# Kernel tuning notes

Hardware: AMD Instinct MI355X
Metric: run time of the kernel (lower is better)

Reference implementation:

```python
import jax, jax.numpy as jnp
import numpy as np


def _pairwise_sq_dist(a, b):
    # a: (B,N,D), b: (B,M,D) -> (B,N,M) squared euclidean distances
    # matmul trick matching torch.cdist (clamped at 0 before implicit sqrt)
    a2 = jnp.sum(a * a, axis=-1)  # (B,N)
    b2 = jnp.sum(b * b, axis=-1)  # (B,M)
    ab = jnp.einsum('bnd,bmd->bnm', a, b)  # (B,N,M)
    d2 = a2[:, :, None] + b2[:, None, :] - 2.0 * ab
    return jnp.maximum(d2, 0.0)


def setup_inputs() -> dict:
    key = jax.random.key(0)
    k1, k2 = jax.random.split(key)
    B, N, M, D = 8, 8192, 8192, 3
    gts = jax.random.normal(k1, (B, N, D), dtype=jnp.float32)
    preds = jax.random.normal(k2, (B, M, D), dtype=jnp.float32)
    return {"gts": gts, "preds": preds}


def reference(gts, preds):
    d2 = _pairwise_sq_dist(gts, preds)           # (B,N,M)
    min_g2p = jnp.min(d2, axis=2)                # (B,N) nearest pred for each gt
    min_p2g = jnp.min(d2, axis=1)                # (B,M) nearest gt for each pred
    return jnp.mean(min_g2p) + jnp.mean(min_p2g)
```

## Files before the change

kernel.cpp:

```cpp
#include <hip/hip_runtime.h>
#include <math.h>

#define BB 8
#define NN 8192
#define MM 8192

#define ROWS_PER_BLOCK 256
#define COLS_PER_BLOCK 1024
#define NTILES (COLS_PER_BLOCK / 32)

typedef __attribute__((ext_vector_type(8)))  short short8;
typedef __attribute__((ext_vector_type(16))) float float16;

#define ONE_BF16 ((short)0x3F80)

__device__ inline unsigned short bf16rn(float f) {
    unsigned int u = __float_as_uint(f);
    u += 0x7FFFu + ((u >> 16) & 1u);
    return (unsigned short)(u >> 16);
}
__device__ inline float bf2f(unsigned short h) {
    return __uint_as_float(((unsigned int)h) << 16);
}
__device__ inline float min16(const float16 d) {
    float v = fminf(fminf(d[0], d[1]), d[2]);
    v = fminf(fminf(v, d[3]),  d[4]);
    v = fminf(fminf(v, d[5]),  d[6]);
    v = fminf(fminf(v, d[7]),  d[8]);
    v = fminf(fminf(v, d[9]),  d[10]);
    v = fminf(fminf(v, d[11]), d[12]);
    v = fminf(fminf(v, d[13]), d[14]);
    return fminf(v, d[15]);
}


__global__ __launch_bounds__(512, 4) void chamfer_main(
    const float* __restrict__ gts, const float* __restrict__ preds,
    unsigned int* __restrict__ minn, unsigned int* __restrict__ minp)
{
    __shared__ short8 sBlo[COLS_PER_BLOCK];
    __shared__ short8 sBhi[COLS_PER_BLOCK];
    __shared__ int colmin[COLS_PER_BLOCK];

    const int b       = blockIdx.z;
    const int rowBase = blockIdx.x * ROWS_PER_BLOCK;
    const int colBase = blockIdx.y * COLS_PER_BLOCK;
    const int tid  = threadIdx.x;
    const int lane = tid & 63;
    const int wave = tid >> 6;
    const int h    = lane >> 5;
    const int c    = lane & 31;

    for (int i = tid; i < COLS_PER_BLOCK; i += 512) {
        const float* p = preds + ((size_t)b * MM + colBase + i) * 3;
        float x = p[0], y = p[1], z = p[2];
        float w = x * x + y * y + z * z;
        unsigned short xh = bf16rn(x), yh = bf16rn(y), zh = bf16rn(z);
        unsigned short xl = bf16rn(x - bf2f(xh));
        unsigned short yl = bf16rn(y - bf2f(yh));
        unsigned short zl = bf16rn(z - bf2f(zh));
        unsigned short wh = bf16rn(w);
        unsigned short wl = bf16rn(w - bf2f(wh));
        short8 lo, hi;
        lo[0]=(short)xh; lo[1]=(short)yh; lo[2]=(short)zh; lo[3]=(short)xl;
        lo[4]=(short)yl; lo[5]=(short)zl; lo[6]=(short)xh; lo[7]=(short)yh;
        hi[0]=(short)zh; hi[1]=ONE_BF16;  hi[2]=ONE_BF16;  hi[3]=(short)wh;
        hi[4]=(short)wl; hi[5]=0;         hi[6]=0;         hi[7]=0;
        sBlo[i] = lo; sBhi[i] = hi;
        colmin[i] = 0x7F800000;
    }

    const float* g = gts + ((size_t)b * NN + rowBase + wave * 32 + c) * 3;
    float gx = g[0], gy = g[1], gz = g[2];
    float gw = gx * gx + gy * gy + gz * gz;
    float mx = -2.0f * gx, my = -2.0f * gy, mz = -2.0f * gz;
    unsigned short axh = bf16rn(mx), ayh = bf16rn(my), azh = bf16rn(mz);
    unsigned short axl = bf16rn(mx - bf2f(axh));
    unsigned short ayl = bf16rn(my - bf2f(ayh));
    unsigned short azl = bf16rn(mz - bf2f(azh));
    unsigned short awh = bf16rn(gw);
    unsigned short awl = bf16rn(gw - bf2f(awh));
    short8 alo, ahi;
    alo[0]=(short)axh; alo[1]=(short)ayh; alo[2]=(short)azh; alo[3]=(short)axh;
    alo[4]=(short)ayh; alo[5]=(short)azh; alo[6]=(short)axl; alo[7]=(short)ayl;
    ahi[0]=(short)azl; ahi[1]=(short)awh; ahi[2]=(short)awl; ahi[3]=ONE_BF16;
    ahi[4]=ONE_BF16;   ahi[5]=0;          ahi[6]=0;          ahi[7]=0;
    short8 afrag = h ? ahi : alo;

    float16 zacc;
#pragma unroll
    for (int q = 0; q < 16; ++q) zacc[q] = 0.0f;

    const float kInf = __builtin_inff();
    float rm[16];
#pragma unroll
    for (int q = 0; q < 16; ++q) rm[q] = kInf;

    __syncthreads();

    const short8* myB = h ? sBhi : sBlo;
    for (int t = 0; t < NTILES; t += 2) {
        short8 b0 = myB[t * 32 + c];
        short8 b1 = myB[(t + 1) * 32 + c];
        float16 d0 = __builtin_amdgcn_mfma_f32_32x32x16_bf16(afrag, b0, zacc, 0, 0, 0);
        float16 d1 = __builtin_amdgcn_mfma_f32_32x32x16_bf16(afrag, b1, zacc, 0, 0, 0);
        atomicMin(&colmin[t * 32 + c],       __float_as_int(min16(d0)));
        atomicMin(&colmin[(t + 1) * 32 + c], __float_as_int(min16(d1)));
#pragma unroll
        for (int q = 0; q < 16; ++q)
            rm[q] = fminf(fminf(rm[q], d0[q]), d1[q]);
    }

#pragma unroll
    for (int q = 0; q < 16; ++q) {
        float v = rm[q];
        v = fminf(v, __shfl_xor(v, 1));
        v = fminf(v, __shfl_xor(v, 2));
        v = fminf(v, __shfl_xor(v, 4));
        v = fminf(v, __shfl_xor(v, 8));
        v = fminf(v, __shfl_xor(v, 16));
        rm[q] = v;
    }
    float sel = rm[0];
#pragma unroll
    for (int q = 1; q < 16; ++q) sel = (c == q) ? rm[q] : sel;
    if (c < 16) {
        int rowInTile = (c & 3) + 8 * (c >> 2) + 4 * h;
        unsigned int bits = __float_as_uint(fmaxf(sel, 0.0f));
        atomicMin(&minn[(size_t)b * NN + rowBase + wave * 32 + rowInTile], bits);
    }

    __syncthreads();
    for (int i = tid; i < COLS_PER_BLOCK; i += 512) {
        unsigned int bits = __float_as_uint(fmaxf(__int_as_float(colmin[i]), 0.0f));
        atomicMin(&minp[(size_t)b * MM + colBase + i], bits);
    }
}

__global__ void chamfer_reduce(const unsigned int* __restrict__ minn,
                               const unsigned int* __restrict__ minp,
                               float* __restrict__ accum,
                               unsigned int* __restrict__ ticket,
                               float* __restrict__ out)
{
    const int idx = blockIdx.x * blockDim.x + threadIdx.x;
    const int stride = gridDim.x * blockDim.x;

    float s0 = 0.0f, s1 = 0.0f;
    for (int i = idx; i < BB * NN; i += stride) s0 += __uint_as_float(minn[i]);
    for (int i = idx; i < BB * MM; i += stride) s1 += __uint_as_float(minp[i]);

#pragma unroll
    for (int m = 1; m < 64; m <<= 1) {
        s0 += __shfl_xor(s0, m, 64);
        s1 += __shfl_xor(s1, m, 64);
    }
    __shared__ float w0[4], w1[4];
    if ((threadIdx.x & 63) == 0) {
        w0[threadIdx.x >> 6] = s0;
        w1[threadIdx.x >> 6] = s1;
    }
    __syncthreads();
    if (threadIdx.x == 0) {
        atomicAdd(&accum[0], w0[0] + w0[1] + w0[2] + w0[3]);
        atomicAdd(&accum[1], w1[0] + w1[1] + w1[2] + w1[3]);
        __threadfence();
        unsigned int old = atomicAdd(ticket, 1u);
        unsigned int G = gridDim.x;
        if (old == 0xAAAAAAAAu + G - 1u || old == G - 1u) {
            float a0 = atomicAdd(&accum[0], 0.0f);
            float a1 = atomicAdd(&accum[1], 0.0f);
            out[0] = a0 / (float)(BB * NN) + a1 / (float)(BB * MM);
        }
    }
}

extern "C" void kernel_launch(void* const* d_in, const int* in_sizes, int n_in,
                              void* d_out, int out_size, void* d_ws, size_t ws_size,
                              hipStream_t stream) {
    const float* gts   = (const float*)d_in[0];
    const float* preds = (const float*)d_in[1];
    float* out = (float*)d_out;

    unsigned int* minn   = (unsigned int*)d_ws;
    unsigned int* minp   = minn + (size_t)BB * NN;
    float*        accum  = (float*)(minp + (size_t)BB * MM);
    unsigned int* ticket = (unsigned int*)(accum + 2);

    dim3 grid(NN / ROWS_PER_BLOCK, MM / COLS_PER_BLOCK, BB);
    chamfer_main<<<grid, 512, 0, stream>>>(gts, preds, minn, minp);

    chamfer_reduce<<<64, 256, 0, stream>>>(minn, minp, accum, ticket, out);
}
```

Measured before the change: 93.80 us.

## Replace row shuffle reduction with LDS atomics, tree min, full unroll, tweak launch

The per-row minimum is now reduced through shared-memory atomicMin into a rowmin array, replacing the 80 cross-lane shuffles per wave. The column min uses a shallower tree of fminf, and the tile loop is fully unrolled. Launch bounds drop from 4 to 2 blocks per SM, giving the compiler more registers, and the reduce kernel launches twice as many blocks. Risks are LDS atomic contention on rowmin, lower occupancy, and more code from the unroll.

```diff
diff --git a/kernel.cpp b/kernel.cpp
--- a/kernel.cpp
+++ b/kernel.cpp
@@ -22,25 +22,26 @@
 __device__ inline float bf2f(unsigned short h) {
     return __uint_as_float(((unsigned int)h) << 16);
 }
-__device__ inline float min16(const float16 d) {
-    float v = fminf(fminf(d[0], d[1]), d[2]);
-    v = fminf(fminf(v, d[3]),  d[4]);
-    v = fminf(fminf(v, d[5]),  d[6]);
-    v = fminf(fminf(v, d[7]),  d[8]);
-    v = fminf(fminf(v, d[9]),  d[10]);
-    v = fminf(fminf(v, d[11]), d[12]);
-    v = fminf(fminf(v, d[13]), d[14]);
-    return fminf(v, d[15]);
+__device__ inline float tree16(const float16 d) {
+    float a = fminf(fminf(d[0],  d[1]),  d[2]);
+    float b = fminf(fminf(d[3],  d[4]),  d[5]);
+    float c = fminf(fminf(d[6],  d[7]),  d[8]);
+    float e = fminf(fminf(d[9],  d[10]), d[11]);
+    float f = fminf(fminf(d[12], d[13]), d[14]);
+    a = fminf(fminf(a, b), c);
+    e = fminf(fminf(e, f), d[15]);
+    return fminf(a, e);
 }
 
 
-__global__ __launch_bounds__(512, 4) void chamfer_main(
+__global__ __launch_bounds__(512, 2) void chamfer_main(
     const float* __restrict__ gts, const float* __restrict__ preds,
     unsigned int* __restrict__ minn, unsigned int* __restrict__ minp)
 {
     __shared__ short8 sBlo[COLS_PER_BLOCK];
     __shared__ short8 sBhi[COLS_PER_BLOCK];
     __shared__ int colmin[COLS_PER_BLOCK];
+    __shared__ int rowmin[ROWS_PER_BLOCK];
 
     const int b       = blockIdx.z;
     const int rowBase = blockIdx.x * ROWS_PER_BLOCK;
@@ -69,6 +70,7 @@
         sBlo[i] = lo; sBhi[i] = hi;
         colmin[i] = 0x7F800000;
     }
+    if (tid < ROWS_PER_BLOCK) rowmin[tid] = 0x7F800000;
 
     const float* g = gts + ((size_t)b * NN + rowBase + wave * 32 + c) * 3;
     float gx = g[0], gy = g[1], gz = g[2];
@@ -99,38 +101,33 @@
     __syncthreads();
 
     const short8* myB = h ? sBhi : sBlo;
+#pragma unroll
     for (int t = 0; t < NTILES; t += 2) {
         short8 b0 = myB[t * 32 + c];
-        short8 b1 = myB[(t + 1) * 32 + c];
+        short8 b1 = myB[t * 32 + 32 + c];
         float16 d0 = __builtin_amdgcn_mfma_f32_32x32x16_bf16(afrag, b0, zacc, 0, 0, 0);
         float16 d1 = __builtin_amdgcn_mfma_f32_32x32x16_bf16(afrag, b1, zacc, 0, 0, 0);
-        atomicMin(&colmin[t * 32 + c],       __float_as_int(min16(d0)));
-        atomicMin(&colmin[(t + 1) * 32 + c], __float_as_int(min16(d1)));
 #pragma unroll
         for (int q = 0; q < 16; ++q)
             rm[q] = fminf(fminf(rm[q], d0[q]), d1[q]);
+        atomicMin(&colmin[t * 32 + c],      __float_as_int(tree16(d0)));
+        atomicMin(&colmin[t * 32 + 32 + c], __float_as_int(tree16(d1)));
     }
 
+    {
+        int* dst = rowmin + wave * 32;
 #pragma unroll
-    for (int q = 0; q < 16; ++q) {
-        float v = rm[q];
-        v = fminf(v, __shfl_xor(v, 1));
-        v = fminf(v, __shfl_xor(v, 2));
-        v = fminf(v, __shfl_xor(v, 4));
-        v = fminf(v, __shfl_xor(v, 8));
-        v = fminf(v, __shfl_xor(v, 16));
-        rm[q] = v;
-    }
-    float sel = rm[0];
-#pragma unroll
-    for (int q = 1; q < 16; ++q) sel = (c == q) ? rm[q] : sel;
-    if (c < 16) {
-        int rowInTile = (c & 3) + 8 * (c >> 2) + 4 * h;
-        unsigned int bits = __float_as_uint(fmaxf(sel, 0.0f));
-        atomicMin(&minn[(size_t)b * NN + rowBase + wave * 32 + rowInTile], bits);
+        for (int q = 0; q < 16; ++q) {
+            int rowInTile = (q & 3) + 8 * (q >> 2) + 4 * h;
+            atomicMin(&dst[rowInTile], __float_as_int(rm[q]));
+        }
     }
 
     __syncthreads();
+    if (tid < ROWS_PER_BLOCK) {
+        unsigned int bits = __float_as_uint(fmaxf(__int_as_float(rowmin[tid]), 0.0f));
+        atomicMin(&minn[(size_t)b * NN + rowBase + tid], bits);
+    }
     for (int i = tid; i < COLS_PER_BLOCK; i += 512) {
         unsigned int bits = __float_as_uint(fmaxf(__int_as_float(colmin[i]), 0.0f));
         atomicMin(&minp[(size_t)b * MM + colBase + i], bits);
@@ -190,5 +187,5 @@
     dim3 grid(NN / ROWS_PER_BLOCK, MM / COLS_PER_BLOCK, BB);
     chamfer_main<<<grid, 512, 0, stream>>>(gts, preds, minn, minp);
 
-    chamfer_reduce<<<64, 256, 0, stream>>>(minn, minp, accum, ticket, out);
+    chamfer_reduce<<<128, 256, 0, stream>>>(minn, minp, accum, ticket, out);
 }
```

After: 136.2 us. +45.2%, slower.
